# Performance work log

Measured on AMD Instinct MI355X. Metric: run time of the kernel, lower is better.

The kernel has to match this reference:

```python
import jax, jax.numpy as jnp
import numpy as np

B, T, D = 1, 2048, 768          # batch, seq_len, d_model
K, V = 8, 1024                   # n_codebooks, vocab_size
D_IN, D_STATE, D_CONV, DT_RANK = 1536, 16, 4, 48  # expand*d_model, ssm state, conv width, dt rank
L, SEG, RET_SCALE = 4, 256, 1.0  # n_layers, segment_size, retrieval_scale


def setup_inputs() -> dict:
    key = jax.random.key(0)
    ks = jax.random.split(key, 12)
    g = lambda k, shape, sc: jax.random.normal(k, shape, jnp.float32) * sc
    tokens = jax.random.randint(ks[0], (B, T, K), 0, V, dtype=jnp.int32)
    return dict(
        tokens=tokens,
        embed_w=g(ks[1], (K, V, D), 0.02),
        W_u=g(ks[2], (L, D, D), 1.0 / np.sqrt(D)),
        in_proj=g(ks[3], (L, 2 * D_IN, D), 1.0 / np.sqrt(D)),
        conv_w=g(ks[4], (L, D_IN, D_CONV), 0.5),
        conv_b=jnp.zeros((L, D_IN), jnp.float32),
        x_proj=g(ks[5], (L, DT_RANK + 2 * D_STATE, D_IN), 1.0 / np.sqrt(D_IN)),
        dt_w=g(ks[6], (L, D_IN, DT_RANK), 1.0 / np.sqrt(DT_RANK)),
        dt_b=jnp.full((L, D_IN), -4.0, jnp.float32),  # softplus(-4) ~ small init dt
        A_log=jnp.log(jnp.broadcast_to(jnp.arange(1.0, D_STATE + 1.0, dtype=jnp.float32), (L, D_IN, D_STATE))),
        D_skip=jnp.ones((L, D_IN), jnp.float32),
        out_proj=g(ks[7], (L, D, D_IN), 1.0 / np.sqrt(D_IN)),
        head_w=g(ks[8], (K, V, D), 0.02),
    )


def _mamba_block(x, in_proj, conv_w, conv_b, x_proj, dt_w, dt_b, A_log, D_skip, out_proj):
    # x: (B, T, D) -> (B, T, D). Canonical Mamba block with selective scan.
    xz = jnp.einsum('btd,ed->bte', x, in_proj)          # (B, T, 2*D_IN)
    u, z = xz[..., :D_IN], xz[..., D_IN:]
    # causal depthwise conv1d, kernel D_CONV
    up = jnp.pad(u, ((0, 0), (D_CONV - 1, 0), (0, 0)))
    u = sum(up[:, k:k + T, :] * conv_w[:, k] for k in range(D_CONV)) + conv_b
    u = jax.nn.silu(u)
    dbc = jnp.einsum('bte,fe->btf', u, x_proj)          # (B, T, DT_RANK + 2*D_STATE)
    dt_low = dbc[..., :DT_RANK]
    Bm = dbc[..., DT_RANK:DT_RANK + D_STATE]
    Cm = dbc[..., DT_RANK + D_STATE:]
    delta = jax.nn.softplus(jnp.einsum('btr,er->bte', dt_low, dt_w) + dt_b)  # (B, T, D_IN)
    A = -jnp.exp(A_log)                                  # (D_IN, D_STATE)

    def step(h, inp):
        d_t, B_t, C_t, u_t = inp                         # (B,D_IN),(B,D_STATE),(B,D_STATE),(B,D_IN)
        dA = jnp.exp(d_t[:, :, None] * A)
        h = dA * h + (d_t * u_t)[:, :, None] * B_t[:, None, :]
        y = jnp.einsum('bes,bs->be', h, C_t)
        return h, y

    h0 = jnp.zeros((B, D_IN, D_STATE), x.dtype)
    xs = (delta.transpose(1, 0, 2), Bm.transpose(1, 0, 2), Cm.transpose(1, 0, 2), u.transpose(1, 0, 2))
    _, ys = jax.lax.scan(jax.checkpoint(step), h0, xs)
    y = ys.transpose(1, 0, 2) + D_skip * u
    y = y * jax.nn.silu(z)
    return jnp.einsum('bte,de->btd', y, out_proj)


def _mc_block(x, W_u_l, mamba_params):
    # Memory-Cached Mamba block: mamba + within-sequence GRM segment retrieval.
    x_out = _mamba_block(x, *mamba_params)
    n_seg = T // SEG
    bpos = (jnp.arange(n_seg) + 1) * SEG - 1
    h_stack = x_out[:, bpos, :]                            # (B, N, D) boundary outputs (values)
    m_stack = x.reshape(B, n_seg, SEG, D).mean(axis=2)     # (B, N, D) segment means of inputs (keys)
    seg_idx = jnp.arange(T) // SEG
    mask = seg_idx[:, None] > jnp.arange(n_seg)[None, :]   # (T, N) causal over segments
    positions = jnp.arange(T)
    seg_starts = (positions // SEG) * SEG
    count = (positions - seg_starts + 1).astype(x.dtype)[None, :, None]
    cs = jnp.cumsum(x, axis=1)
    padded = jnp.concatenate([jnp.zeros((B, 1, D), x.dtype), cs], axis=1)
    m_current = (cs - padded[:, seg_starts, :]) / count    # running within-segment mean
    scale = 1.0 / np.sqrt(D)
    u = jnp.einsum('btd,ed->bte', x, W_u_l)
    sc = jnp.einsum('btd,bnd->btn', u, m_stack) * scale
    sc = jnp.where(mask[None], sc, -1e30)
    s_cur = jnp.sum(u * m_current, axis=-1, keepdims=True) * scale
    attn = jax.nn.softmax(jnp.concatenate([sc, s_cur], axis=-1), axis=-1)  # (B, T, N+1)
    h_ret = jnp.einsum('btn,bnd->btd', attn[..., :n_seg], h_stack)
    gate_cur = attn[..., n_seg:]
    return gate_cur * x_out + RET_SCALE * h_ret


def reference(tokens, embed_w, W_u, in_proj, conv_w, conv_b, x_proj, dt_w, dt_b, A_log, D_skip, out_proj, head_w):
    # RVQ embedding: sum of per-codebook embeddings
    x = embed_w[jnp.arange(K), tokens].sum(axis=2)         # (B, T, D)
    for l in range(L):
        mp = (in_proj[l], conv_w[l], conv_b[l], x_proj[l], dt_w[l], dt_b[l], A_log[l], D_skip[l], out_proj[l])
        x = _mc_block(x, W_u[l], mp)
    return jnp.einsum('btd,kvd->btkv', x, head_w)          # (B, T, K, V) per-codebook logits
```

## Files before the change

### kernel.cpp

```cpp
#include <hip/hip_runtime.h>
#include <hip/hip_bf16.h>


#define T_LEN   2048
#define DMODEL  768
#define DIN     1536
#define DXZ     3072
#define NSTATE  16
#define DTRANK  48
#define FDIM    80
#define NSEG    8
#define SEGLEN  256
#define NHEADV  8192
#define CH      64
#define NC      32

#define OFF_X     0u
#define OFF_XZ    1572864u
#define OFF_UC    7864320u
#define OFF_DBC   11010048u
#define OFF_DELTA 11173888u
#define OFF_Y     14319616u
#define OFF_XOUT  17465344u
#define OFF_URET  19038208u
#define OFF_MCUR  20611072u
#define OFF_MSTK  22183936u
#define OFF_WEMB  22190080u
#define OFF_WCW   28481536u
#define OFF_WCB   28506112u
#define OFF_WXP   28512256u
#define OFF_WDW   29003776u
#define OFF_WDB   29298688u
#define OFF_WAL   29304832u
#define OFF_WDS   29403136u
#define OFF_SLOC  29409280u
#define OFF_HIN   30195712u
#define OFF_CHP   30982144u
#define WS_TOTAL  31031296u
__device__ __align__(16) float g_ws[WS_TOTAL];

#define BF_XHI   0u
#define BF_XLO   1572864u
#define BF_YHI   3145728u
#define BF_YLO   6291456u
#define BF_IPHI  9437184u
#define BF_IPLO  18874368u
#define BF_OPHI  28311552u
#define BF_OPLO  33030144u
#define BF_WUHI  37748736u
#define BF_WULO  40108032u
#define BF_HWHI  42467328u
#define BF_HWLO  48758784u
#define BF_TOTAL 55050240u
__device__ __align__(16) unsigned short g_bf[BF_TOTAL];
__device__ unsigned int g_isbf16;

typedef __attribute__((ext_vector_type(8))) short bf16x8;
typedef __attribute__((ext_vector_type(4))) float f32x4;

__device__ __forceinline__ float bf2f(unsigned short u) {
  union { unsigned int i; float f; } c; c.i = ((unsigned int)u) << 16; return c.f;
}
__device__ __forceinline__ unsigned short f2bf(float f) {
  union { float f; unsigned int i; } c; c.f = f;
  unsigned int lsb = (c.i >> 16) & 1u;
  unsigned int r = c.i + 0x7fffu + lsb;
  return (unsigned short)(r >> 16);
}
__device__ __forceinline__ float softplusf(float v) {
  return v > 0.f ? v + log1pf(expf(-v)) : log1pf(expf(v));
}

__device__ __forceinline__ void gload16(const unsigned short* g, unsigned short* l) {
  __builtin_amdgcn_global_load_lds(
      (__attribute__((address_space(1))) unsigned int*)(unsigned long long)g,
      (__attribute__((address_space(3))) unsigned int*)(unsigned int)(unsigned long long)l,
      16, 0, 0);
}

__global__ void detect_kernel(const unsigned int* __restrict__ dsk) {
  if (threadIdx.x == 0 && blockIdx.x == 0)
    g_isbf16 = (dsk[0] == 0x3F803F80u) ? 1u : 0u;
}

__global__ __launch_bounds__(256) void convert_kernel(
    const void* __restrict__ src, unsigned int dstoff, int n) {
  int stride = gridDim.x * 256;
  bool isb = (g_isbf16 != 0u);
  for (int i = blockIdx.x * 256 + threadIdx.x; i < n; i += stride) {
    float v = isb ? bf2f(((const unsigned short*)src)[i])
                  : ((const float*)src)[i];
    g_ws[dstoff + i] = v;
  }
}

__global__ __launch_bounds__(256) void splitw_kernel(
    const void* __restrict__ src, unsigned hioff, unsigned looff, int n) {
  int stride = gridDim.x * 256;
  bool isb = (g_isbf16 != 0u);
  for (int i = blockIdx.x * 256 + threadIdx.x; i < n; i += stride) {
    float v = isb ? bf2f(((const unsigned short*)src)[i])
                  : ((const float*)src)[i];
    unsigned short h = f2bf(v);
    g_bf[hioff + i] = h;
    g_bf[looff + i] = f2bf(v - bf2f(h));
  }
}

__global__ __launch_bounds__(256) void split_act(
    unsigned srcoff, unsigned hioff, unsigned looff, int n) {
  int i = blockIdx.x * 256 + threadIdx.x;
  if (i >= n) return;
  float v = g_ws[srcoff + i];
  unsigned short h = f2bf(v);
  g_bf[hioff + i] = h;
  g_bf[looff + i] = f2bf(v - bf2f(h));
}

__global__ __launch_bounds__(256) void embed_kernel(const int* __restrict__ tokens) {
  int t = blockIdx.x;
  int tid = threadIdx.x;
  const float* __restrict__ emb = g_ws + OFF_WEMB;
  int tok[8];
#pragma unroll
  for (int k = 0; k < 8; ++k) tok[k] = tokens[t * 8 + k];
#pragma unroll
  for (int j = 0; j < 3; ++j) {
    int d = tid + j * 256;
    float s = 0.f;
#pragma unroll
    for (int k = 0; k < 8; ++k)
      s += emb[((size_t)k * 1024 + tok[k]) * DMODEL + d];
    g_ws[OFF_X + (size_t)t * DMODEL + d] = s;
  }
}

template <int BN, int EPI>
__global__ __launch_bounds__(256) void gemm_mfma(
    unsigned ahio, unsigned aloo, unsigned whio, unsigned wloo,
    unsigned coff, void* __restrict__ Cout, int ldc, int K) {
  constexpr int NWH = BN / 16;
  constexpr int NCH = 16 + 2 * NWH;
  constexpr int MI  = (BN == 128) ? 4 : 2;
  __shared__ __align__(16) unsigned short sA[2][128 * 32];
  __shared__ __align__(16) unsigned short sW[2][BN * 32];
  const unsigned short* __restrict__ ahi = g_bf + ahio;
  const unsigned short* __restrict__ alo = g_bf + aloo;
  const unsigned short* __restrict__ whi = g_bf + whio;
  const unsigned short* __restrict__ wlo = g_bf + wloo;
  int tid = threadIdx.x;
  int w = tid >> 6, lane = tid & 63;
  int lm = lane & 15, quad = lane >> 4;
  int bm = blockIdx.y * 128, bn = blockIdx.x * BN;
  int wr = (BN == 128) ? ((w >> 1) * 64) : (w * 32);
  int wc = (BN == 128) ? ((w & 1) * 64) : 0;
  int srow = lane >> 2;
  int scol = (lane & 3) * 8;
  f32x4 acc[MI][4] = {};
  for (int k0 = 0; k0 < K; k0 += 32) {
#pragma unroll
    for (int ci = 0; ci < NCH / 4; ++ci) {
      int ch = w + ci * 4;
      const unsigned short* src;
      unsigned short* dst;
      if (ch < 8) {
        src = ahi + (size_t)(bm + ch * 16 + srow) * K + k0 + scol;
        dst = &sA[0][ch * 512];
      } else if (ch < 16) {
        src = alo + (size_t)(bm + (ch - 8) * 16 + srow) * K + k0 + scol;
        dst = &sA[1][(ch - 8) * 512];
      } else if (ch < 16 + NWH) {
        src = whi + (size_t)(bn + (ch - 16) * 16 + srow) * K + k0 + scol;
        dst = &sW[0][(ch - 16) * 512];
      } else {
        src = wlo + (size_t)(bn + (ch - 16 - NWH) * 16 + srow) * K + k0 + scol;
        dst = &sW[1][(ch - 16 - NWH) * 512];
      }
      gload16(src, dst);
    }
    __syncthreads();
    bf16x8 ah[MI], al[MI], wh[4], wl[4];
#pragma unroll
    for (int mi = 0; mi < MI; ++mi) {
      int r = wr + mi * 16 + lm;
      ah[mi] = *(const bf16x8*)&sA[0][r * 32 + quad * 8];
      al[mi] = *(const bf16x8*)&sA[1][r * 32 + quad * 8];
    }
#pragma unroll
    for (int ni = 0; ni < 4; ++ni) {
      int r = wc + ni * 16 + lm;
      wh[ni] = *(const bf16x8*)&sW[0][r * 32 + quad * 8];
      wl[ni] = *(const bf16x8*)&sW[1][r * 32 + quad * 8];
    }
#pragma unroll
    for (int mi = 0; mi < MI; ++mi)
#pragma unroll
      for (int ni = 0; ni < 4; ++ni) {
        acc[mi][ni] = __builtin_amdgcn_mfma_f32_16x16x32_bf16(ah[mi], wh[ni], acc[mi][ni], 0, 0, 0);
        acc[mi][ni] = __builtin_amdgcn_mfma_f32_16x16x32_bf16(ah[mi], wl[ni], acc[mi][ni], 0, 0, 0);
        acc[mi][ni] = __builtin_amdgcn_mfma_f32_16x16x32_bf16(al[mi], wh[ni], acc[mi][ni], 0, 0, 0);
      }
    __syncthreads();
  }
  bool outb = (EPI == 2) && (g_isbf16 != 0u);
#pragma unroll
  for (int mi = 0; mi < MI; ++mi)
#pragma unroll
    for (int ni = 0; ni < 4; ++ni)
#pragma unroll
      for (int r = 0; r < 4; ++r) {
        int gm = bm + wr + mi * 16 + quad * 4 + r;
        int gn = bn + wc + ni * 16 + lm;
        float v = acc[mi][ni][r];
        if (EPI == 2) {
          if (outb) ((unsigned short*)Cout)[(size_t)gm * ldc + gn] = f2bf(v);
          else      ((float*)Cout)[(size_t)gm * ldc + gn] = v;
        } else {
          g_ws[coff + (size_t)gm * ldc + gn] = v;
        }
      }
}

template <int EPI>
__global__ __launch_bounds__(256) void gemm_nt(
    unsigned int aoff, int lda, unsigned int boff, int ldb,
    unsigned int coff, int ldc, int M, int N, int K, unsigned int biasoff) {
  const float* __restrict__ A = g_ws + aoff;
  const float* __restrict__ Bw = g_ws + boff;
  __shared__ float As[16][68];
  __shared__ float Bs[16][68];
  int tid = threadIdx.x;
  int bx = blockIdx.x, by = blockIdx.y;
  int tx = tid & 15, ty = tid >> 4;
  int lr = tid >> 2;
  int lc = (tid & 3) * 4;
  float acc[4][4] = {};
  for (int k0 = 0; k0 < K; k0 += 16) {
    const float* ap = A + (size_t)(by * 64 + lr) * lda + k0 + lc;
    float4 av = *reinterpret_cast<const float4*>(ap);
    As[lc + 0][lr] = av.x; As[lc + 1][lr] = av.y;
    As[lc + 2][lr] = av.z; As[lc + 3][lr] = av.w;
    int bn = bx * 64 + lr;
    float4 bv = make_float4(0.f, 0.f, 0.f, 0.f);
    if (bn < N)
      bv = *reinterpret_cast<const float4*>(Bw + (size_t)bn * ldb + k0 + lc);
    Bs[lc + 0][lr] = bv.x; Bs[lc + 1][lr] = bv.y;
    Bs[lc + 2][lr] = bv.z; Bs[lc + 3][lr] = bv.w;
    __syncthreads();
#pragma unroll
    for (int kk = 0; kk < 16; ++kk) {
      float4 a = *reinterpret_cast<const float4*>(&As[kk][ty * 4]);
      float4 b = *reinterpret_cast<const float4*>(&Bs[kk][tx * 4]);
      float ar[4] = {a.x, a.y, a.z, a.w};
      float br[4] = {b.x, b.y, b.z, b.w};
#pragma unroll
      for (int i = 0; i < 4; ++i)
#pragma unroll
        for (int j = 0; j < 4; ++j) acc[i][j] = fmaf(ar[i], br[j], acc[i][j]);
    }
    __syncthreads();
  }
  int m0 = by * 64 + ty * 4, n0 = bx * 64 + tx * 4;
#pragma unroll
  for (int i = 0; i < 4; ++i) {
#pragma unroll
    for (int j = 0; j < 4; ++j) {
      int m = m0 + i, n = n0 + j;
      if (n < N) {
        float v = acc[i][j];
        if (EPI == 1) v = softplusf(v + g_ws[biasoff + n]);
        g_ws[coff + (size_t)m * ldc + n] = v;
      }
    }
  }
}

__global__ __launch_bounds__(256) void conv_silu_kernel(
    unsigned int cwoff, unsigned int cboff) {
  int idx = blockIdx.x * 256 + threadIdx.x;
  int t = idx / DIN, e = idx - t * DIN;
  const float* __restrict__ xz = g_ws + OFF_XZ;
  const float* __restrict__ cw = g_ws + cwoff;
  float w0 = cw[e * 4 + 0], w1 = cw[e * 4 + 1];
  float w2 = cw[e * 4 + 2], w3 = cw[e * 4 + 3];
  float acc = g_ws[cboff + e];
  if (t >= 3) acc = fmaf(w0, xz[(size_t)(t - 3) * DXZ + e], acc);
  if (t >= 2) acc = fmaf(w1, xz[(size_t)(t - 2) * DXZ + e], acc);
  if (t >= 1) acc = fmaf(w2, xz[(size_t)(t - 1) * DXZ + e], acc);
  acc = fmaf(w3, xz[(size_t)t * DXZ + e], acc);
  float sig = 1.f / (1.f + __expf(-acc));
  g_ws[OFF_UC + idx] = acc * sig;
}

__global__ __launch_bounds__(256) void scan_phase1(unsigned int aloff) {
  int tid = threadIdx.x;
  int s = tid & 15;
  int e = blockIdx.x * 16 + (tid >> 4);
  int c = blockIdx.y;
  int t0 = c * CH;
  const float* __restrict__ delta = g_ws + OFF_DELTA;
  const float* __restrict__ uc    = g_ws + OFF_UC;
  const float* __restrict__ dbc   = g_ws + OFF_DBC;
  float a = -expf(g_ws[aloff + e * NSTATE + s]);
  float h = 0.f, P = 0.f;
  for (int i = 0; i < CH; ++i) {
    int t = t0 + i;
    float d = delta[(size_t)t * DIN + e];
    float u = uc[(size_t)t * DIN + e];
    float b = dbc[t * FDIM + DTRANK + s];
    float cc = dbc[t * FDIM + DTRANK + NSTATE + s];
    float dA = __expf(d * a);
    h = fmaf(dA, h, d * u * b);
    P += d;
    float yp = h * cc;
    yp += __shfl_xor(yp, 1);
    yp += __shfl_xor(yp, 2);
    yp += __shfl_xor(yp, 4);
    yp += __shfl_xor(yp, 8);
    if (s == 0) g_ws[OFF_Y + (size_t)t * DIN + e] = yp;
  }
  g_ws[OFF_SLOC + ((size_t)c * DIN + e) * NSTATE + s] = h;
  if (s == 0) g_ws[OFF_CHP + c * DIN + e] = P;
}

__global__ __launch_bounds__(256) void scan_phase2(unsigned int aloff) {
  int g = blockIdx.x * 256 + threadIdx.x;
  int e = g >> 4, s = g & 15;
  float a = -expf(g_ws[aloff + e * NSTATE + s]);
  float h = 0.f;
  for (int c = 0; c < NC; ++c) {
    g_ws[OFF_HIN + ((size_t)c * DIN + e) * NSTATE + s] = h;
    float S = g_ws[OFF_SLOC + ((size_t)c * DIN + e) * NSTATE + s];
    float P = g_ws[OFF_CHP + c * DIN + e];
    h = fmaf(__expf(a * P), h, S);
  }
}

__global__ __launch_bounds__(256) void scan_phase3(unsigned int aloff,
                                                   unsigned int dsoff) {
  int tid = threadIdx.x;
  int s = tid & 15;
  int e = blockIdx.x * 16 + (tid >> 4);
  int c = blockIdx.y;
  int t0 = c * CH;
  const float* __restrict__ delta = g_ws + OFF_DELTA;
  const float* __restrict__ uc    = g_ws + OFF_UC;
  const float* __restrict__ dbc   = g_ws + OFF_DBC;
  const float* __restrict__ xz    = g_ws + OFF_XZ;
  float a = -expf(g_ws[aloff + e * NSTATE + s]);
  float dsk = g_ws[dsoff + e];
  float hin = g_ws[OFF_HIN + ((size_t)c * DIN + e) * NSTATE + s];
  float P = 0.f;
  for (int i = 0; i < CH; ++i) {
    int t = t0 + i;
    float d = delta[(size_t)t * DIN + e];
    P += d;
    float cc = dbc[t * FDIM + DTRANK + NSTATE + s];
    float yp = __expf(a * P) * hin * cc;
    yp += __shfl_xor(yp, 1);
    yp += __shfl_xor(yp, 2);
    yp += __shfl_xor(yp, 4);
    yp += __shfl_xor(yp, 8);
    if (s == 0) {
      float u = uc[(size_t)t * DIN + e];
      float z = xz[(size_t)t * DXZ + DIN + e];
      float y = g_ws[OFF_Y + (size_t)t * DIN + e] + yp;
      float sig = 1.f / (1.f + __expf(-z));
      g_ws[OFF_Y + (size_t)t * DIN + e] = (y + dsk * u) * z * sig;
    }
  }
}

__global__ __launch_bounds__(256) void mcurrent_kernel() {
  int n = blockIdx.x / 3;
  int d = (blockIdx.x % 3) * 256 + threadIdx.x;
  const float* __restrict__ x = g_ws + OFF_X + (size_t)n * SEGLEN * DMODEL + d;
  float* __restrict__ mc = g_ws + OFF_MCUR + (size_t)n * SEGLEN * DMODEL + d;
  float run = 0.f;
  for (int i = 0; i < SEGLEN; ++i) {
    run += x[(size_t)i * DMODEL];
    mc[(size_t)i * DMODEL] = run / (float)(i + 1);
  }
}

__global__ __launch_bounds__(256) void retention_kernel() {
  int t = blockIdx.x;
  int tid = threadIdx.x;
  const float* __restrict__ xout = g_ws + OFF_XOUT;
  const float* __restrict__ uret = g_ws + OFF_URET;
  const float* __restrict__ mcur = g_ws + OFF_MCUR;
  __shared__ float red[4][9];
  __shared__ float attn_s[9];
  float p[9];
#pragma unroll
  for (int n = 0; n < 9; ++n) p[n] = 0.f;
#pragma unroll
  for (int j = 0; j < 3; ++j) {
    int d = tid + j * 256;
    float u = uret[(size_t)t * DMODEL + d];
    p[8] = fmaf(u, mcur[(size_t)t * DMODEL + d], p[8]);
#pragma unroll
    for (int n = 0; n < 8; ++n)
      p[n] = fmaf(u, mcur[(size_t)(n * SEGLEN + SEGLEN - 1) * DMODEL + d], p[n]);
  }
#pragma unroll
  for (int off = 32; off > 0; off >>= 1)
#pragma unroll
    for (int n = 0; n < 9; ++n) p[n] += __shfl_down(p[n], off, 64);
  int wave = tid >> 6;
  if ((tid & 63) == 0)
#pragma unroll
    for (int n = 0; n < 9; ++n) red[wave][n] = p[n];
  __syncthreads();
  if (tid == 0) {
    const float scale = 0.03608439182435161f;
    int seg = t >> 8;
    float sc[9], mx = -3.0e38f;
#pragma unroll
    for (int n = 0; n < 9; ++n) {
      float v = (red[0][n] + red[1][n] + red[2][n] + red[3][n]) * scale;
      if (n < 8 && n >= seg) v = -1e30f;
      sc[n] = v;
      mx = fmaxf(mx, v);
    }
    float den = 0.f;
#pragma unroll
    for (int n = 0; n < 9; ++n) {
      float e = __expf(sc[n] - mx);
      sc[n] = e;
      den += e;
    }
    float inv = 1.f / den;
#pragma unroll
    for (int n = 0; n < 9; ++n) attn_s[n] = sc[n] * inv;
  }
  __syncthreads();
  float a[9];
#pragma unroll
  for (int n = 0; n < 9; ++n) a[n] = attn_s[n];
#pragma unroll
  for (int j = 0; j < 3; ++j) {
    int d = tid + j * 256;
    float acc = a[8] * xout[(size_t)t * DMODEL + d];
#pragma unroll
    for (int n = 0; n < 8; ++n)
      acc = fmaf(a[n], xout[(size_t)(n * SEGLEN + SEGLEN - 1) * DMODEL + d], acc);
    g_ws[OFF_X + (size_t)t * DMODEL + d] = acc;
  }
}

extern "C" void kernel_launch(void* const* d_in, const int* in_sizes, int n_in,
                              void* d_out, int out_size, void* d_ws, size_t ws_size,
                              hipStream_t stream) {
  (void)in_sizes; (void)n_in; (void)out_size; (void)d_ws; (void)ws_size;
  const int* tokens = (const int*)d_in[0];

  detect_kernel<<<1, 64, 0, stream>>>((const unsigned int*)d_in[10]);

  struct { int idx; unsigned int off; int n; } conv_list[8] = {
    { 1, OFF_WEMB, 8 * 1024 * 768 },
    { 4, OFF_WCW,  4 * 1536 * 4 },
    { 5, OFF_WCB,  4 * 1536 },
    { 6, OFF_WXP,  4 * 80 * 1536 },
    { 7, OFF_WDW,  4 * 1536 * 48 },
    { 8, OFF_WDB,  4 * 1536 },
    { 9, OFF_WAL,  4 * 1536 * 16 },
    {10, OFF_WDS,  4 * 1536 },
  };
  for (int i = 0; i < 8; ++i) {
    int blocks = (conv_list[i].n + 255) / 256;
    if (blocks > 4096) blocks = 4096;
    convert_kernel<<<blocks, 256, 0, stream>>>(d_in[conv_list[i].idx],
                                               conv_list[i].off, conv_list[i].n);
  }
  splitw_kernel<<<4096, 256, 0, stream>>>(d_in[3],  BF_IPHI, BF_IPLO, 4 * 3072 * 768);
  splitw_kernel<<<4096, 256, 0, stream>>>(d_in[11], BF_OPHI, BF_OPLO, 4 * 768 * 1536);
  splitw_kernel<<<4096, 256, 0, stream>>>(d_in[2],  BF_WUHI, BF_WULO, 4 * 768 * 768);
  splitw_kernel<<<4096, 256, 0, stream>>>(d_in[12], BF_HWHI, BF_HWLO, 8192 * 768);

  embed_kernel<<<T_LEN, 256, 0, stream>>>(tokens);

  for (int l = 0; l < 4; ++l) {
    unsigned int xp = OFF_WXP + (unsigned)l * FDIM * DIN;
    unsigned int dw = OFF_WDW + (unsigned)l * DIN * DTRANK;
    unsigned int db = OFF_WDB + (unsigned)l * DIN;
    unsigned int al = OFF_WAL + (unsigned)l * DIN * NSTATE;
    unsigned int ds = OFF_WDS + (unsigned)l * DIN;
    unsigned int cw = OFF_WCW + (unsigned)l * DIN * 4;
    unsigned int cb = OFF_WCB + (unsigned)l * DIN;
    unsigned int iphi = BF_IPHI + (unsigned)l * DXZ * DMODEL;
    unsigned int iplo = BF_IPLO + (unsigned)l * DXZ * DMODEL;
    unsigned int ophi = BF_OPHI + (unsigned)l * DMODEL * DIN;
    unsigned int oplo = BF_OPLO + (unsigned)l * DMODEL * DIN;
    unsigned int wuhi = BF_WUHI + (unsigned)l * DMODEL * DMODEL;
    unsigned int wulo = BF_WULO + (unsigned)l * DMODEL * DMODEL;

    split_act<<<(T_LEN * DMODEL) / 256, 256, 0, stream>>>(OFF_X, BF_XHI, BF_XLO,
                                                          T_LEN * DMODEL);
    gemm_mfma<128, 0><<<dim3(DXZ / 128, T_LEN / 128), 256, 0, stream>>>(
        BF_XHI, BF_XLO, iphi, iplo, OFF_XZ, nullptr, DXZ, DMODEL);
    conv_silu_kernel<<<(T_LEN * DIN) / 256, 256, 0, stream>>>(cw, cb);
    gemm_nt<0><<<dim3(2, 32), 256, 0, stream>>>(OFF_UC, DIN, xp, DIN,
                                                OFF_DBC, FDIM, T_LEN, FDIM, DIN, 0u);
    gemm_nt<1><<<dim3(24, 32), 256, 0, stream>>>(OFF_DBC, FDIM, dw, DTRANK,
                                                 OFF_DELTA, DIN, T_LEN, DIN, DTRANK, db);
    scan_phase1<<<dim3(DIN / 16, NC), 256, 0, stream>>>(al);
    scan_phase2<<<(DIN * NSTATE) / 256, 256, 0, stream>>>(al);
    scan_phase3<<<dim3(DIN / 16, NC), 256, 0, stream>>>(al, ds);
    split_act<<<(T_LEN * DIN) / 256, 256, 0, stream>>>(OFF_Y, BF_YHI, BF_YLO,
                                                       T_LEN * DIN);
    gemm_mfma<64, 0><<<dim3(DMODEL / 64, T_LEN / 128), 256, 0, stream>>>(
        BF_YHI, BF_YLO, ophi, oplo, OFF_XOUT, nullptr, DMODEL, DIN);
    mcurrent_kernel<<<NSEG * 3, 256, 0, stream>>>();
    gemm_mfma<64, 0><<<dim3(DMODEL / 64, T_LEN / 128), 256, 0, stream>>>(
        BF_XHI, BF_XLO, wuhi, wulo, OFF_URET, nullptr, DMODEL, DMODEL);
    retention_kernel<<<T_LEN, 256, 0, stream>>>();
  }

  split_act<<<(T_LEN * DMODEL) / 256, 256, 0, stream>>>(OFF_X, BF_XHI, BF_XLO,
                                                        T_LEN * DMODEL);
  gemm_mfma<128, 2><<<dim3(NHEADV / 128, T_LEN / 128), 256, 0, stream>>>(
      BF_XHI, BF_XLO, BF_HWHI, BF_HWLO, 0u, d_out, NHEADV, DMODEL);
}
```

Before: 2.446 ms.

## Double-buffer GEMM LDS tiles and merge weight conversion launches

The MFMA GEMM now double-buffers its LDS tiles, issuing the async global-to-LDS loads for the next K step before computing on the current one, with one barrier per iteration. The LDS staging layout changes so each 16-row chunk is stored lane-contiguous, so fragment reads become simple lane*8 offsets. The eight convert launches and four split-weight launches are merged into two flat kernels to cut launch overhead. LDS use doubles, which may reduce occupancy.

```diff
diff --git a/kernel.cpp b/kernel.cpp
--- a/kernel.cpp
+++ b/kernel.cpp
@@ -83,28 +83,42 @@
     g_isbf16 = (dsk[0] == 0x3F803F80u) ? 1u : 0u;
 }
 
-__global__ __launch_bounds__(256) void convert_kernel(
-    const void* __restrict__ src, unsigned int dstoff, int n) {
-  int stride = gridDim.x * 256;
+__global__ __launch_bounds__(256) void convert_all(
+    const void* __restrict__ s0, const void* __restrict__ s1,
+    const void* __restrict__ s2, const void* __restrict__ s3,
+    const void* __restrict__ s4, const void* __restrict__ s5,
+    const void* __restrict__ s6, const void* __restrict__ s7) {
+  int i = blockIdx.x * 256 + threadIdx.x;
+  if (i >= 7219200) return;
   bool isb = (g_isbf16 != 0u);
-  for (int i = blockIdx.x * 256 + threadIdx.x; i < n; i += stride) {
-    float v = isb ? bf2f(((const unsigned short*)src)[i])
-                  : ((const float*)src)[i];
-    g_ws[dstoff + i] = v;
-  }
-}
-
-__global__ __launch_bounds__(256) void splitw_kernel(
-    const void* __restrict__ src, unsigned hioff, unsigned looff, int n) {
-  int stride = gridDim.x * 256;
+  const void* src; unsigned dst; int j;
+  if      (i < 6291456) { src = s0; dst = OFF_WEMB; j = i; }
+  else if (i < 6316032) { src = s1; dst = OFF_WCW;  j = i - 6291456; }
+  else if (i < 6322176) { src = s2; dst = OFF_WCB;  j = i - 6316032; }
+  else if (i < 6813696) { src = s3; dst = OFF_WXP;  j = i - 6322176; }
+  else if (i < 7108608) { src = s4; dst = OFF_WDW;  j = i - 6813696; }
+  else if (i < 7114752) { src = s5; dst = OFF_WDB;  j = i - 7108608; }
+  else if (i < 7213056) { src = s6; dst = OFF_WAL;  j = i - 7114752; }
+  else                  { src = s7; dst = OFF_WDS;  j = i - 7213056; }
+  float v = isb ? bf2f(((const unsigned short*)src)[j]) : ((const float*)src)[j];
+  g_ws[dst + j] = v;
+}
+
+__global__ __launch_bounds__(256) void splitw_all(
+    const void* __restrict__ s0, const void* __restrict__ s1,
+    const void* __restrict__ s2, const void* __restrict__ s3) {
+  int i = blockIdx.x * 256 + threadIdx.x;
+  if (i >= 22806528) return;
   bool isb = (g_isbf16 != 0u);
-  for (int i = blockIdx.x * 256 + threadIdx.x; i < n; i += stride) {
-    float v = isb ? bf2f(((const unsigned short*)src)[i])
-                  : ((const float*)src)[i];
-    unsigned short h = f2bf(v);
-    g_bf[hioff + i] = h;
-    g_bf[looff + i] = f2bf(v - bf2f(h));
-  }
+  const void* src; unsigned hi, lo; int j;
+  if      (i <  9437184) { src = s0; hi = BF_IPHI; lo = BF_IPLO; j = i; }
+  else if (i < 14155776) { src = s1; hi = BF_OPHI; lo = BF_OPLO; j = i - 9437184; }
+  else if (i < 16515072) { src = s2; hi = BF_WUHI; lo = BF_WULO; j = i - 14155776; }
+  else                   { src = s3; hi = BF_HWHI; lo = BF_HWLO; j = i - 16515072; }
+  float v = isb ? bf2f(((const unsigned short*)src)[j]) : ((const float*)src)[j];
+  unsigned short h = f2bf(v);
+  g_bf[hi + j] = h;
+  g_bf[lo + j] = f2bf(v - bf2f(h));
 }
 
 __global__ __launch_bounds__(256) void split_act(
@@ -142,8 +156,8 @@
   constexpr int NWH = BN / 16;
   constexpr int NCH = 16 + 2 * NWH;
   constexpr int MI  = (BN == 128) ? 4 : 2;
-  __shared__ __align__(16) unsigned short sA[2][128 * 32];
-  __shared__ __align__(16) unsigned short sW[2][BN * 32];
+  __shared__ __align__(16) unsigned short sA[2][2][128 * 32];
+  __shared__ __align__(16) unsigned short sW[2][2][BN * 32];
   const unsigned short* __restrict__ ahi = g_bf + ahio;
   const unsigned short* __restrict__ alo = g_bf + aloo;
   const unsigned short* __restrict__ whi = g_bf + whio;
@@ -154,10 +168,11 @@
   int bm = blockIdx.y * 128, bn = blockIdx.x * BN;
   int wr = (BN == 128) ? ((w >> 1) * 64) : (w * 32);
   int wc = (BN == 128) ? ((w & 1) * 64) : 0;
-  int srow = lane >> 2;
-  int scol = (lane & 3) * 8;
+  int srow = lane & 15;
+  int scol = (lane >> 4) * 8;
   f32x4 acc[MI][4] = {};
-  for (int k0 = 0; k0 < K; k0 += 32) {
+
+  auto stage = [&](int k0, int b) {
 #pragma unroll
     for (int ci = 0; ci < NCH / 4; ++ci) {
       int ch = w + ci * 4;
@@ -165,32 +180,38 @@
       unsigned short* dst;
       if (ch < 8) {
         src = ahi + (size_t)(bm + ch * 16 + srow) * K + k0 + scol;
-        dst = &sA[0][ch * 512];
+        dst = &sA[b][0][ch * 512];
       } else if (ch < 16) {
         src = alo + (size_t)(bm + (ch - 8) * 16 + srow) * K + k0 + scol;
-        dst = &sA[1][(ch - 8) * 512];
+        dst = &sA[b][1][(ch - 8) * 512];
       } else if (ch < 16 + NWH) {
         src = whi + (size_t)(bn + (ch - 16) * 16 + srow) * K + k0 + scol;
-        dst = &sW[0][(ch - 16) * 512];
+        dst = &sW[b][0][(ch - 16) * 512];
       } else {
         src = wlo + (size_t)(bn + (ch - 16 - NWH) * 16 + srow) * K + k0 + scol;
-        dst = &sW[1][(ch - 16 - NWH) * 512];
+        dst = &sW[b][1][(ch - 16 - NWH) * 512];
       }
       gload16(src, dst);
     }
-    __syncthreads();
+  };
+
+  int nk = K >> 5;
+  stage(0, 0);
+  __syncthreads();
+  int cur = 0;
+  int cA = wr >> 4, cW = wc >> 4;
+  for (int t = 0; t < nk; ++t) {
+    if (t + 1 < nk) stage((t + 1) << 5, cur ^ 1);
     bf16x8 ah[MI], al[MI], wh[4], wl[4];
 #pragma unroll
     for (int mi = 0; mi < MI; ++mi) {
-      int r = wr + mi * 16 + lm;
-      ah[mi] = *(const bf16x8*)&sA[0][r * 32 + quad * 8];
-      al[mi] = *(const bf16x8*)&sA[1][r * 32 + quad * 8];
+      ah[mi] = *(const bf16x8*)&sA[cur][0][(cA + mi) * 512 + lane * 8];
+      al[mi] = *(const bf16x8*)&sA[cur][1][(cA + mi) * 512 + lane * 8];
     }
 #pragma unroll
     for (int ni = 0; ni < 4; ++ni) {
-      int r = wc + ni * 16 + lm;
-      wh[ni] = *(const bf16x8*)&sW[0][r * 32 + quad * 8];
-      wl[ni] = *(const bf16x8*)&sW[1][r * 32 + quad * 8];
+      wh[ni] = *(const bf16x8*)&sW[cur][0][(cW + ni) * 512 + lane * 8];
+      wl[ni] = *(const bf16x8*)&sW[cur][1][(cW + ni) * 512 + lane * 8];
     }
 #pragma unroll
     for (int mi = 0; mi < MI; ++mi)
@@ -201,7 +222,9 @@
         acc[mi][ni] = __builtin_amdgcn_mfma_f32_16x16x32_bf16(al[mi], wh[ni], acc[mi][ni], 0, 0, 0);
       }
     __syncthreads();
-  }
+    cur ^= 1;
+  }
+
   bool outb = (EPI == 2) && (g_isbf16 != 0u);
 #pragma unroll
   for (int mi = 0; mi < MI; ++mi)
@@ -457,26 +480,10 @@
 
   detect_kernel<<<1, 64, 0, stream>>>((const unsigned int*)d_in[10]);
 
-  struct { int idx; unsigned int off; int n; } conv_list[8] = {
-    { 1, OFF_WEMB, 8 * 1024 * 768 },
-    { 4, OFF_WCW,  4 * 1536 * 4 },
-    { 5, OFF_WCB,  4 * 1536 },
-    { 6, OFF_WXP,  4 * 80 * 1536 },
-    { 7, OFF_WDW,  4 * 1536 * 48 },
-    { 8, OFF_WDB,  4 * 1536 },
-    { 9, OFF_WAL,  4 * 1536 * 16 },
-    {10, OFF_WDS,  4 * 1536 },
-  };
-  for (int i = 0; i < 8; ++i) {
-    int blocks = (conv_list[i].n + 255) / 256;
-    if (blocks > 4096) blocks = 4096;
-    convert_kernel<<<blocks, 256, 0, stream>>>(d_in[conv_list[i].idx],
-                                               conv_list[i].off, conv_list[i].n);
-  }
-  splitw_kernel<<<4096, 256, 0, stream>>>(d_in[3],  BF_IPHI, BF_IPLO, 4 * 3072 * 768);
-  splitw_kernel<<<4096, 256, 0, stream>>>(d_in[11], BF_OPHI, BF_OPLO, 4 * 768 * 1536);
-  splitw_kernel<<<4096, 256, 0, stream>>>(d_in[2],  BF_WUHI, BF_WULO, 4 * 768 * 768);
-  splitw_kernel<<<4096, 256, 0, stream>>>(d_in[12], BF_HWHI, BF_HWLO, 8192 * 768);
+  convert_all<<<(7219200 + 255) / 256, 256, 0, stream>>>(
+      d_in[1], d_in[4], d_in[5], d_in[6], d_in[7], d_in[8], d_in[9], d_in[10]);
+  splitw_all<<<(22806528 + 255) / 256, 256, 0, stream>>>(
+      d_in[3], d_in[11], d_in[2], d_in[12]);
 
   embed_kernel<<<T_LEN, 256, 0, stream>>>(tokens);
 
```

New measurement: 2.498 ms. 1.02x slower.
